# Performance work log

Hardware: AMD Instinct MI355X
Metric: run time of the kernel (lower is better)

The kernel has to match this reference:

```python
import jax, jax.numpy as jnp
import numpy as np

H = 1024      # hidden_size
NH = 16       # num_heads
HD = H // NH  # head_dim


def setup_inputs() -> dict:
    key = jax.random.key(0)
    ks = jax.random.split(key, 5)
    x = jax.random.normal(ks[0], (2, 2048, H), dtype=jnp.float32)
    # nn.Linear weights are [out, in]; keep that convention
    w_qkv = jax.random.normal(ks[1], (3 * H, H), dtype=jnp.float32) * (1.0 / np.sqrt(H))
    b_qkv = jax.random.normal(ks[2], (3 * H,), dtype=jnp.float32) * 0.01
    w_out = jax.random.normal(ks[3], (H, H), dtype=jnp.float32) * (1.0 / np.sqrt(H))
    b_out = jax.random.normal(ks[4], (H,), dtype=jnp.float32) * 0.01
    return {"x": x, "w_qkv": w_qkv, "b_qkv": b_qkv, "w_out": w_out, "b_out": b_out}


def reference(x, w_qkv, b_qkv, w_out, b_out):
    B, L, _ = x.shape
    scale = HD ** -0.5
    qkv = x @ w_qkv.T + b_qkv                       # [B,L,3H]
    qkv = qkv.reshape(B, L, 3, NH, HD).transpose(2, 0, 3, 1, 4)  # [3,B,NH,L,HD]
    q, k, v = qkv[0], qkv[1], qkv[2]
    attn = jnp.einsum('bhqd,bhkd->bhqk', q, k) * scale
    attn = jax.nn.softmax(attn, axis=-1)            # dropout is identity in eval
    out = jnp.einsum('bhqk,bhkd->bhqd', attn, v)    # [B,NH,L,HD]
    out = out.transpose(0, 2, 1, 3).reshape(B, L, H)
    return out @ w_out.T + b_out
```

## Files before the change

### kernel.cpp

```cpp
#include <hip/hip_runtime.h>
#include <hip/hip_bf16.h>
#include <stdint.h>

#define H_DIM  1024
#define NHEADS 16
#define HDIM   64
#define BATCH  2
#define SEQ    2048
#define MROWS  (BATCH * SEQ)
#define QKV_N  (3 * H_DIM)
#define QK_LD  (2 * H_DIM)
#define NT     (SEQ / 64)

typedef __attribute__((ext_vector_type(8))) __bf16 bf16x8;
typedef __attribute__((ext_vector_type(4))) float  floatx4;

__device__ __forceinline__ unsigned short f2bf(float f) {
    uint32_t u = __float_as_uint(f);
    u += 0x7fffu + ((u >> 16) & 1u);
    return (unsigned short)(u >> 16);
}
__device__ __forceinline__ float bf2f(unsigned short u) {
    return __uint_as_float(((uint32_t)u) << 16);
}
__device__ __forceinline__ uint32_t cvtpk_bf16(float lo, float hi) {
    uint32_t r;
    asm("v_cvt_pk_bf16_f32 %0, %1, %2" : "=v"(r) : "v"(lo), "v"(hi));
    return r;
}

__device__ __forceinline__ void async_ld16(const void* g, void* l) {
    __builtin_amdgcn_global_load_lds(
        (const __attribute__((address_space(1))) void*)g,
        (__attribute__((address_space(3))) void*)l, 16, 0, 0);
}

__global__ __launch_bounds__(256) void cvt_f32_bf16(const float4* __restrict__ in,
                                                    ushort4* __restrict__ out, int n4) {
    int i = blockIdx.x * 256 + threadIdx.x;
    if (i < n4) {
        float4 v = in[i];
        ushort4 o;
        o.x = f2bf(v.x); o.y = f2bf(v.y); o.z = f2bf(v.z); o.w = f2bf(v.w);
        out[i] = o;
    }
}

__global__ __launch_bounds__(256) void gemm_bt(const unsigned short* __restrict__ A,
                                               const unsigned short* __restrict__ B,
                                               const float* __restrict__ bias,
                                               unsigned short* __restrict__ Cb,
                                               float* __restrict__ Cf,
                                               unsigned short* __restrict__ Vt,
                                               int ldc, int Kdim) {
    __shared__ __align__(16) unsigned short As[128 * 32];
    __shared__ __align__(16) unsigned short Bs[128 * 32];
    const int tid  = threadIdx.x;
    const int lane = tid & 63;
    const int wave = tid >> 6;
    const int waveM = (wave >> 1) * 64;
    const int waveN = (wave & 1) * 64;
    const int bm = blockIdx.y, bn = blockIdx.x;

    floatx4 acc[4][4];
    #pragma unroll
    for (int i = 0; i < 4; ++i)
        #pragma unroll
        for (int j = 0; j < 4; ++j) {
            floatx4 z = {0.f, 0.f, 0.f, 0.f};
            acc[i][j] = z;
        }

    const int c0 = tid, c1 = tid + 256;
    const int r0 = c0 >> 2, kc0 = (c0 & 3) * 8;
    const int r1 = c1 >> 2, kc1 = (c1 & 3) * 8;
    char* asb0 = (char*)As + wave * 1024;
    char* asb1 = (char*)As + 4096 + wave * 1024;
    char* bsb0 = (char*)Bs + wave * 1024;
    char* bsb1 = (char*)Bs + 4096 + wave * 1024;

    const int lr = lane & 15;
    const int lk = (lane >> 4) * 8;

    for (int k0 = 0; k0 < Kdim; k0 += 32) {
        async_ld16(&A[(size_t)(bm * 128 + r0) * Kdim + k0 + kc0], asb0);
        async_ld16(&A[(size_t)(bm * 128 + r1) * Kdim + k0 + kc1], asb1);
        async_ld16(&B[(size_t)(bn * 128 + r0) * Kdim + k0 + kc0], bsb0);
        async_ld16(&B[(size_t)(bn * 128 + r1) * Kdim + k0 + kc1], bsb1);
        __syncthreads();

        bf16x8 af[4], bfr[4];
        #pragma unroll
        for (int i = 0; i < 4; ++i)
            af[i] = *(const bf16x8*)&As[(waveM + i * 16 + lr) * 32 + lk];
        #pragma unroll
        for (int j = 0; j < 4; ++j)
            bfr[j] = *(const bf16x8*)&Bs[(waveN + j * 16 + lr) * 32 + lk];

        #pragma unroll
        for (int i = 0; i < 4; ++i)
            #pragma unroll
            for (int j = 0; j < 4; ++j)
                acc[i][j] = __builtin_amdgcn_mfma_f32_16x16x32_bf16(af[i], bfr[j], acc[i][j], 0, 0, 0);
        __syncthreads();
    }

    const int crow0 = bm * 128 + waveM + (lane >> 4) * 4;
    const int ccol0 = bn * 128 + waveN + (lane & 15);
    #pragma unroll
    for (int i = 0; i < 4; ++i)
        #pragma unroll
        for (int j = 0; j < 4; ++j) {
            int col = ccol0 + j * 16;
            float bv = bias[col];
            #pragma unroll
            for (int r = 0; r < 4; ++r) {
                int row = crow0 + i * 16 + r;
                float v = acc[i][j][r] + bv;
                if (Vt && col >= 2 * H_DIM) {
                    int hd = col - 2 * H_DIM;
                    int bb = row >> 11, kv = row & (SEQ - 1);
                    int hh = hd >> 6,  dd = hd & 63;
                    Vt[((size_t)((bb << 4) + hh) * HDIM + dd) * SEQ + kv] = f2bf(v);
                } else if (Cb) {
                    Cb[(size_t)row * ldc + col] = f2bf(v);
                } else {
                    Cf[(size_t)row * ldc + col] = v;
                }
            }
        }
}

__global__ __launch_bounds__(256) void gemm_bt64(const unsigned short* __restrict__ A,
                                                 const unsigned short* __restrict__ B,
                                                 const float* __restrict__ bias,
                                                 float* __restrict__ Cf,
                                                 int ldc, int Kdim) {
    __shared__ __align__(16) unsigned short As[128 * 32];
    __shared__ __align__(16) unsigned short Bs[64 * 32];
    const int tid  = threadIdx.x;
    const int lane = tid & 63;
    const int wave = tid >> 6;
    const int waveM = wave * 32;
    const int bm = blockIdx.y, bn = blockIdx.x;

    floatx4 acc[2][4];
    #pragma unroll
    for (int i = 0; i < 2; ++i)
        #pragma unroll
        for (int j = 0; j < 4; ++j) {
            floatx4 z = {0.f, 0.f, 0.f, 0.f};
            acc[i][j] = z;
        }

    const int c0 = tid, c1 = tid + 256;
    const int r0 = c0 >> 2, kc0 = (c0 & 3) * 8;
    const int r1 = c1 >> 2, kc1 = (c1 & 3) * 8;
    char* asb0 = (char*)As + wave * 1024;
    char* asb1 = (char*)As + 4096 + wave * 1024;
    char* bsb0 = (char*)Bs + wave * 1024;

    const int lr = lane & 15;
    const int lk = (lane >> 4) * 8;

    for (int k0 = 0; k0 < Kdim; k0 += 32) {
        async_ld16(&A[(size_t)(bm * 128 + r0) * Kdim + k0 + kc0], asb0);
        async_ld16(&A[(size_t)(bm * 128 + r1) * Kdim + k0 + kc1], asb1);
        async_ld16(&B[(size_t)(bn * 64 + r0) * Kdim + k0 + kc0], bsb0);
        __syncthreads();

        bf16x8 af[2], bfr[4];
        #pragma unroll
        for (int i = 0; i < 2; ++i)
            af[i] = *(const bf16x8*)&As[(waveM + i * 16 + lr) * 32 + lk];
        #pragma unroll
        for (int j = 0; j < 4; ++j)
            bfr[j] = *(const bf16x8*)&Bs[(j * 16 + lr) * 32 + lk];

        #pragma unroll
        for (int i = 0; i < 2; ++i)
            #pragma unroll
            for (int j = 0; j < 4; ++j)
                acc[i][j] = __builtin_amdgcn_mfma_f32_16x16x32_bf16(af[i], bfr[j], acc[i][j], 0, 0, 0);
        __syncthreads();
    }

    const int crow0 = bm * 128 + waveM + (lane >> 4) * 4;
    const int ccol0 = bn * 64 + (lane & 15);
    #pragma unroll
    for (int i = 0; i < 2; ++i)
        #pragma unroll
        for (int j = 0; j < 4; ++j) {
            int col = ccol0 + j * 16;
            float bv = bias[col];
            #pragma unroll
            for (int r = 0; r < 4; ++r) {
                int row = crow0 + i * 16 + r;
                Cf[(size_t)row * ldc + col] = acc[i][j][r] + bv;
            }
        }
}

__global__ __launch_bounds__(256, 4) void attn_mfma(const unsigned short* __restrict__ qkv2,
                                                    const unsigned short* __restrict__ vt,
                                                    unsigned short* __restrict__ ctx) {
    __shared__ __align__(16) unsigned short Ks2[2][64 * 64];
    __shared__ __align__(16) unsigned short Vt2[2][64 * 64];

    const int tid  = threadIdx.x;
    const int lane = tid & 63;
    const int wave = tid >> 6;
    const int bh = blockIdx.y;
    const int b  = bh >> 4, h = bh & 15;
    const int q0 = blockIdx.x * 64 + wave * 16;
    const int lq = lane & 15;
    const int g  = lane >> 4;
    const int swz = lq & 7;

    const float QS = 0.125f * 1.44269504f;
    bf16x8 qf[2];
    #pragma unroll
    for (int kk = 0; kk < 2; ++kk) {
        union { bf16x8 v; unsigned short u[8]; } tq;
        tq.v = *(const bf16x8*)&qkv2[(size_t)(b * SEQ + q0 + lq) * QK_LD
                                     + h * HDIM + kk * 32 + g * 8];
        #pragma unroll
        for (int e = 0; e < 8; ++e) tq.u[e] = f2bf(bf2f(tq.u[e]) * QS);
        qf[kk] = tq.v;
    }

    floatx4 acc_o[4];
    #pragma unroll
    for (int j = 0; j < 4; ++j) {
        floatx4 z = {0.f, 0.f, 0.f, 0.f};
        acc_o[j] = z;
    }
    float l_run = 0.f;

    const unsigned short* gK = qkv2 + (size_t)b * SEQ * QK_LD + H_DIM + (size_t)h * HDIM;
    const unsigned short* gV = vt + (size_t)bh * HDIM * SEQ;

    const int r0  = tid >> 3;
    const int pr0 = (r0 & 32) | ((r0 & 12) << 1) | ((r0 & 16) >> 2) | (r0 & 3);
    const int gs0 = (tid & 7) ^ (r0 & 7);
    const unsigned short* pK0 = gK + (size_t)pr0 * QK_LD + gs0 * 8;
    const unsigned short* pK1 = gK + (size_t)(pr0 + 32) * QK_LD + gs0 * 8;
    const unsigned short* pV0 = gV + (size_t)r0 * SEQ + gs0 * 8;
    const unsigned short* pV1 = gV + (size_t)(r0 + 32) * SEQ + gs0 * 8;

    #define STAGE_KV(bi)                                                        \
        {                                                                       \
            async_ld16(pK0, (char*)&Ks2[bi][0] + (wave * 64) * 16);             \
            async_ld16(pK1, (char*)&Ks2[bi][0] + (256 + wave * 64) * 16);       \
            async_ld16(pV0, (char*)&Vt2[bi][0] + (wave * 64) * 16);             \
            async_ld16(pV1, (char*)&Vt2[bi][0] + (256 + wave * 64) * 16);       \
            pK0 += 64 * QK_LD; pK1 += 64 * QK_LD; pV0 += 64; pV1 += 64;         \
        }

    STAGE_KV(0)
    __syncthreads();

    int buf = 0;
    for (int t = 0; t < NT; ++t) {
        if (t + 1 < NT) STAGE_KV(buf ^ 1)

        const unsigned short* Ksb = &Ks2[buf][0];
        const unsigned short* Vsb = &Vt2[buf][0];

        bf16x8 kf[4][2];
        #pragma unroll
        for (int jb = 0; jb < 4; ++jb)
            #pragma unroll
            for (int kk = 0; kk < 2; ++kk)
                kf[jb][kk] = *(const bf16x8*)&Ksb[(jb * 16 + lq) * 64 + (((kk << 2) + g) ^ swz) * 8];

        bf16x8 vf[4][2];
        #pragma unroll
        for (int dt = 0; dt < 4; ++dt)
            #pragma unroll
            for (int kk = 0; kk < 2; ++kk)
                vf[dt][kk] = *(const bf16x8*)&Vsb[(dt * 16 + lq) * 64 + (((kk << 2) + g) ^ swz) * 8];

        __builtin_amdgcn_sched_barrier(0);

        floatx4 sa[4];
        #pragma unroll
        for (int jb = 0; jb < 4; ++jb) {
            floatx4 z = {0.f, 0.f, 0.f, 0.f};
            sa[jb] = z;
        }
        __builtin_amdgcn_s_setprio(1);
        #pragma unroll
        for (int jb = 0; jb < 4; ++jb)
            #pragma unroll
            for (int kk = 0; kk < 2; ++kk)
                sa[jb] = __builtin_amdgcn_mfma_f32_16x16x32_bf16(kf[jb][kk], qf[kk], sa[jb], 0, 0, 0);
        __builtin_amdgcn_s_setprio(0);

        float ps = 0.f;

        {
            float e00 = exp2f(sa[0][0]), e01 = exp2f(sa[0][1]), e02 = exp2f(sa[0][2]), e03 = exp2f(sa[0][3]);
            float e10 = exp2f(sa[1][0]), e11 = exp2f(sa[1][1]), e12 = exp2f(sa[1][2]), e13 = exp2f(sa[1][3]);
            ps += ((e00 + e01) + (e02 + e03)) + ((e10 + e11) + (e12 + e13));
            union { bf16x8 v; uint32_t u[4]; } pf;
            pf.u[0] = cvtpk_bf16(e00, e01); pf.u[1] = cvtpk_bf16(e02, e03);
            pf.u[2] = cvtpk_bf16(e10, e11); pf.u[3] = cvtpk_bf16(e12, e13);
            __builtin_amdgcn_s_setprio(1);
            #pragma unroll
            for (int dt = 0; dt < 4; ++dt)
                acc_o[dt] = __builtin_amdgcn_mfma_f32_16x16x32_bf16(pf.v, vf[dt][0], acc_o[dt], 0, 0, 0);
            __builtin_amdgcn_s_setprio(0);
        }

        {
            float e00 = exp2f(sa[2][0]), e01 = exp2f(sa[2][1]), e02 = exp2f(sa[2][2]), e03 = exp2f(sa[2][3]);
            float e10 = exp2f(sa[3][0]), e11 = exp2f(sa[3][1]), e12 = exp2f(sa[3][2]), e13 = exp2f(sa[3][3]);
            ps += ((e00 + e01) + (e02 + e03)) + ((e10 + e11) + (e12 + e13));
            union { bf16x8 v; uint32_t u[4]; } pf;
            pf.u[0] = cvtpk_bf16(e00, e01); pf.u[1] = cvtpk_bf16(e02, e03);
            pf.u[2] = cvtpk_bf16(e10, e11); pf.u[3] = cvtpk_bf16(e12, e13);
            __builtin_amdgcn_s_setprio(1);
            #pragma unroll
            for (int dt = 0; dt < 4; ++dt)
                acc_o[dt] = __builtin_amdgcn_mfma_f32_16x16x32_bf16(pf.v, vf[dt][1], acc_o[dt], 0, 0, 0);
            __builtin_amdgcn_s_setprio(0);
        }

        ps += __shfl_xor(ps, 16);
        ps += __shfl_xor(ps, 32);
        l_run += ps;

        __syncthreads();
        buf ^= 1;
    }
    #undef STAGE_KV

    float linv[4];
    #pragma unroll
    for (int r = 0; r < 4; ++r)
        linv[r] = 1.f / __shfl(l_run, g * 4 + r);
    #pragma unroll
    for (int dt = 0; dt < 4; ++dt)
        #pragma unroll
        for (int r = 0; r < 4; ++r)
            ctx[(size_t)(b * SEQ + q0 + g * 4 + r) * H_DIM + h * HDIM + dt * 16 + lq]
                = f2bf(acc_o[dt][r] * linv[r]);
}

extern "C" void kernel_launch(void* const* d_in, const int* in_sizes, int n_in,
                              void* d_out, int out_size, void* d_ws, size_t ws_size,
                              hipStream_t stream) {
    const float* x     = (const float*)d_in[0];
    const float* w_qkv = (const float*)d_in[1];
    const float* b_qkv = (const float*)d_in[2];
    const float* w_out = (const float*)d_in[3];
    const float* b_out = (const float*)d_in[4];
    float* out = (float*)d_out;

    unsigned short* xb    = (unsigned short*)d_ws;
    unsigned short* wqkvb = xb    + (size_t)MROWS * H_DIM;
    unsigned short* woutb = wqkvb + (size_t)QKV_N * H_DIM;
    unsigned short* qkv2  = woutb + (size_t)H_DIM * H_DIM;
    unsigned short* ctxb  = qkv2  + (size_t)MROWS * QK_LD;
    unsigned short* vtb   = ctxb  + (size_t)MROWS * H_DIM;

    cvt_f32_bf16<<<MROWS * H_DIM / 1024, 256, 0, stream>>>((const float4*)x,     (ushort4*)xb,    MROWS * H_DIM / 4);
    cvt_f32_bf16<<<QKV_N * H_DIM / 1024, 256, 0, stream>>>((const float4*)w_qkv, (ushort4*)wqkvb, QKV_N * H_DIM / 4);
    cvt_f32_bf16<<<H_DIM * H_DIM / 1024, 256, 0, stream>>>((const float4*)w_out, (ushort4*)woutb, H_DIM * H_DIM / 4);

    gemm_bt<<<dim3(QKV_N / 128, MROWS / 128), 256, 0, stream>>>(xb, wqkvb, b_qkv, qkv2, nullptr, vtb, QK_LD, H_DIM);

    attn_mfma<<<dim3(SEQ / 64, BATCH * NHEADS), 256, 0, stream>>>(qkv2, vtb, ctxb);

    gemm_bt64<<<dim3(H_DIM / 64, MROWS / 128), 256, 0, stream>>>(ctxb, woutb, b_out, out, H_DIM, H_DIM);
}
```

Baseline: 219.0 us.

## Double GEMM K-tile to 64 with XOR-swizzled LDS and raw exp2 intrinsic

Both GEMM kernels now stage 64-wide K slices per iteration instead of 32, which halves the number of barrier pairs per K loop and issues more MFMAs between syncs. The LDS layout is XOR-swizzled on 16-byte chunks by row so the wider fragment reads avoid bank conflicts. The attention softmax switches from exp2f to the raw hardware exp2 builtin when available, dropping range-handling code. LDS use per block doubles, which may lower occupancy, and the raw exp2 drops denormal handling.

```diff
diff --git a/kernel.cpp b/kernel.cpp
--- a/kernel.cpp
+++ b/kernel.cpp
@@ -29,6 +29,12 @@
     return r;
 }
 
+#if __has_builtin(__builtin_amdgcn_exp2f)
+#define fexp2 __builtin_amdgcn_exp2f
+#else
+#define fexp2 exp2f
+#endif
+
 __device__ __forceinline__ void async_ld16(const void* g, void* l) {
     __builtin_amdgcn_global_load_lds(
         (const __attribute__((address_space(1))) void*)g,
@@ -53,8 +59,8 @@
                                                float* __restrict__ Cf,
                                                unsigned short* __restrict__ Vt,
                                                int ldc, int Kdim) {
-    __shared__ __align__(16) unsigned short As[128 * 32];
-    __shared__ __align__(16) unsigned short Bs[128 * 32];
+    __shared__ __align__(16) unsigned short As[128 * 64];
+    __shared__ __align__(16) unsigned short Bs[128 * 64];
     const int tid  = threadIdx.x;
     const int lane = tid & 63;
     const int wave = tid >> 6;
@@ -71,37 +77,45 @@
             acc[i][j] = z;
         }
 
-    const int c0 = tid, c1 = tid + 256;
-    const int r0 = c0 >> 2, kc0 = (c0 & 3) * 8;
-    const int r1 = c1 >> 2, kc1 = (c1 & 3) * 8;
-    char* asb0 = (char*)As + wave * 1024;
-    char* asb1 = (char*)As + 4096 + wave * 1024;
-    char* bsb0 = (char*)Bs + wave * 1024;
-    char* bsb1 = (char*)Bs + 4096 + wave * 1024;
+    int rr[4], kc[4];
+    #pragma unroll
+    for (int i = 0; i < 4; ++i) {
+        int c = i * 256 + tid;
+        rr[i] = c >> 3;
+        kc[i] = ((c & 7) ^ (rr[i] & 7)) * 8;
+    }
 
     const int lr = lane & 15;
-    const int lk = (lane >> 4) * 8;
-
-    for (int k0 = 0; k0 < Kdim; k0 += 32) {
-        async_ld16(&A[(size_t)(bm * 128 + r0) * Kdim + k0 + kc0], asb0);
-        async_ld16(&A[(size_t)(bm * 128 + r1) * Kdim + k0 + kc1], asb1);
-        async_ld16(&B[(size_t)(bn * 128 + r0) * Kdim + k0 + kc0], bsb0);
-        async_ld16(&B[(size_t)(bn * 128 + r1) * Kdim + k0 + kc1], bsb1);
+    const int g  = lane >> 4;
+    const int sw = lr & 7;
+
+    for (int k0 = 0; k0 < Kdim; k0 += 64) {
+        #pragma unroll
+        for (int i = 0; i < 4; ++i) {
+            async_ld16(&A[(size_t)(bm * 128 + rr[i]) * Kdim + k0 + kc[i]],
+                       (char*)As + i * 4096 + wave * 1024);
+            async_ld16(&B[(size_t)(bn * 128 + rr[i]) * Kdim + k0 + kc[i]],
+                       (char*)Bs + i * 4096 + wave * 1024);
+        }
         __syncthreads();
 
-        bf16x8 af[4], bfr[4];
-        #pragma unroll
-        for (int i = 0; i < 4; ++i)
-            af[i] = *(const bf16x8*)&As[(waveM + i * 16 + lr) * 32 + lk];
-        #pragma unroll
-        for (int j = 0; j < 4; ++j)
-            bfr[j] = *(const bf16x8*)&Bs[(waveN + j * 16 + lr) * 32 + lk];
-
-        #pragma unroll
-        for (int i = 0; i < 4; ++i)
+        #pragma unroll
+        for (int kk = 0; kk < 2; ++kk) {
+            const int gk = (((kk << 2) + g) ^ sw) * 8;
+            bf16x8 af[4], bfr[4];
+            #pragma unroll
+            for (int i = 0; i < 4; ++i)
+                af[i] = *(const bf16x8*)&As[(waveM + i * 16 + lr) * 64 + gk];
             #pragma unroll
             for (int j = 0; j < 4; ++j)
-                acc[i][j] = __builtin_amdgcn_mfma_f32_16x16x32_bf16(af[i], bfr[j], acc[i][j], 0, 0, 0);
+                bfr[j] = *(const bf16x8*)&Bs[(waveN + j * 16 + lr) * 64 + gk];
+
+            #pragma unroll
+            for (int i = 0; i < 4; ++i)
+                #pragma unroll
+                for (int j = 0; j < 4; ++j)
+                    acc[i][j] = __builtin_amdgcn_mfma_f32_16x16x32_bf16(af[i], bfr[j], acc[i][j], 0, 0, 0);
+        }
         __syncthreads();
     }
 
@@ -136,8 +150,8 @@
                                                  const float* __restrict__ bias,
                                                  float* __restrict__ Cf,
                                                  int ldc, int Kdim) {
-    __shared__ __align__(16) unsigned short As[128 * 32];
-    __shared__ __align__(16) unsigned short Bs[64 * 32];
+    __shared__ __align__(16) unsigned short As[128 * 64];
+    __shared__ __align__(16) unsigned short Bs[64 * 64];
     const int tid  = threadIdx.x;
     const int lane = tid & 63;
     const int wave = tid >> 6;
@@ -153,35 +167,46 @@
             acc[i][j] = z;
         }
 
-    const int c0 = tid, c1 = tid + 256;
-    const int r0 = c0 >> 2, kc0 = (c0 & 3) * 8;
-    const int r1 = c1 >> 2, kc1 = (c1 & 3) * 8;
-    char* asb0 = (char*)As + wave * 1024;
-    char* asb1 = (char*)As + 4096 + wave * 1024;
-    char* bsb0 = (char*)Bs + wave * 1024;
+    int rr[4], kc[4];
+    #pragma unroll
+    for (int i = 0; i < 4; ++i) {
+        int c = i * 256 + tid;
+        rr[i] = c >> 3;
+        kc[i] = ((c & 7) ^ (rr[i] & 7)) * 8;
+    }
 
     const int lr = lane & 15;
-    const int lk = (lane >> 4) * 8;
-
-    for (int k0 = 0; k0 < Kdim; k0 += 32) {
-        async_ld16(&A[(size_t)(bm * 128 + r0) * Kdim + k0 + kc0], asb0);
-        async_ld16(&A[(size_t)(bm * 128 + r1) * Kdim + k0 + kc1], asb1);
-        async_ld16(&B[(size_t)(bn * 64 + r0) * Kdim + k0 + kc0], bsb0);
+    const int g  = lane >> 4;
+    const int sw = lr & 7;
+
+    for (int k0 = 0; k0 < Kdim; k0 += 64) {
+        #pragma unroll
+        for (int i = 0; i < 4; ++i)
+            async_ld16(&A[(size_t)(bm * 128 + rr[i]) * Kdim + k0 + kc[i]],
+                       (char*)As + i * 4096 + wave * 1024);
+        #pragma unroll
+        for (int i = 0; i < 2; ++i)
+            async_ld16(&B[(size_t)(bn * 64 + rr[i]) * Kdim + k0 + kc[i]],
+                       (char*)Bs + i * 4096 + wave * 1024);
         __syncthreads();
 
-        bf16x8 af[2], bfr[4];
-        #pragma unroll
-        for (int i = 0; i < 2; ++i)
-            af[i] = *(const bf16x8*)&As[(waveM + i * 16 + lr) * 32 + lk];
-        #pragma unroll
-        for (int j = 0; j < 4; ++j)
-            bfr[j] = *(const bf16x8*)&Bs[(j * 16 + lr) * 32 + lk];
-
-        #pragma unroll
-        for (int i = 0; i < 2; ++i)
+        #pragma unroll
+        for (int kk = 0; kk < 2; ++kk) {
+            const int gk = (((kk << 2) + g) ^ sw) * 8;
+            bf16x8 af[2], bfr[4];
+            #pragma unroll
+            for (int i = 0; i < 2; ++i)
+                af[i] = *(const bf16x8*)&As[(waveM + i * 16 + lr) * 64 + gk];
             #pragma unroll
             for (int j = 0; j < 4; ++j)
-                acc[i][j] = __builtin_amdgcn_mfma_f32_16x16x32_bf16(af[i], bfr[j], acc[i][j], 0, 0, 0);
+                bfr[j] = *(const bf16x8*)&Bs[(j * 16 + lr) * 64 + gk];
+
+            #pragma unroll
+            for (int i = 0; i < 2; ++i)
+                #pragma unroll
+                for (int j = 0; j < 4; ++j)
+                    acc[i][j] = __builtin_amdgcn_mfma_f32_16x16x32_bf16(af[i], bfr[j], acc[i][j], 0, 0, 0);
+        }
         __syncthreads();
     }
 
@@ -300,8 +325,8 @@
         float ps = 0.f;
 
         {
-            float e00 = exp2f(sa[0][0]), e01 = exp2f(sa[0][1]), e02 = exp2f(sa[0][2]), e03 = exp2f(sa[0][3]);
-            float e10 = exp2f(sa[1][0]), e11 = exp2f(sa[1][1]), e12 = exp2f(sa[1][2]), e13 = exp2f(sa[1][3]);
+            float e00 = fexp2(sa[0][0]), e01 = fexp2(sa[0][1]), e02 = fexp2(sa[0][2]), e03 = fexp2(sa[0][3]);
+            float e10 = fexp2(sa[1][0]), e11 = fexp2(sa[1][1]), e12 = fexp2(sa[1][2]), e13 = fexp2(sa[1][3]);
             ps += ((e00 + e01) + (e02 + e03)) + ((e10 + e11) + (e12 + e13));
             union { bf16x8 v; uint32_t u[4]; } pf;
             pf.u[0] = cvtpk_bf16(e00, e01); pf.u[1] = cvtpk_bf16(e02, e03);
@@ -314,8 +339,8 @@
         }
 
         {
-            float e00 = exp2f(sa[2][0]), e01 = exp2f(sa[2][1]), e02 = exp2f(sa[2][2]), e03 = exp2f(sa[2][3]);
-            float e10 = exp2f(sa[3][0]), e11 = exp2f(sa[3][1]), e12 = exp2f(sa[3][2]), e13 = exp2f(sa[3][3]);
+            float e00 = fexp2(sa[2][0]), e01 = fexp2(sa[2][1]), e02 = fexp2(sa[2][2]), e03 = fexp2(sa[2][3]);
+            float e10 = fexp2(sa[3][0]), e11 = fexp2(sa[3][1]), e12 = fexp2(sa[3][2]), e13 = fexp2(sa[3][3]);
             ps += ((e00 + e01) + (e02 + e03)) + ((e10 + e11) + (e12 + e13));
             union { bf16x8 v; uint32_t u[4]; } pf;
             pf.u[0] = cvtpk_bf16(e00, e01); pf.u[1] = cvtpk_bf16(e02, e03);
```

After: 194.7 us. -11.1%, faster.
